# Kernel tuning notes

Measured on AMD Instinct MI355X. Metric: run time of the kernel, lower is better.

## Reference

```python
import jax, jax.numpy as jnp
import numpy as np

N_QUBITS = 4
N_LAYERS = 3
DIM = 2 ** N_QUBITS  # 16
BATCH = 524288

# CNOT ring permutations: wire 0 is the MOST significant bit (PennyLane default.qubit).
# CNOT(c,t) maps basis index j -> j ^ (target_mask * control_bit(j)); it is its own inverse,
# so new_state[:, j] = old_state[:, perm[j]] with the same perm.
_idx = np.arange(DIM)

def _cnot_perm(c, t):
    cbit = (_idx >> (N_QUBITS - 1 - c)) & 1
    return _idx ^ (cbit << (N_QUBITS - 1 - t))

CNOT_PERMS = [jnp.asarray(_cnot_perm(i, (i + 1) % N_QUBITS)) for i in range(N_QUBITS)]

# PauliZ signs per wire: +1 if bit is 0, -1 if bit is 1. Shape (4, 16).
Z_SIGNS = jnp.asarray(
    np.stack([1.0 - 2.0 * ((_idx >> (N_QUBITS - 1 - w)) & 1) for w in range(N_QUBITS)]).astype(np.float32)
)


def _bcast(v):
    # angle-derived factor: scalar stays scalar, batched (B,) -> (B,1,1)
    return v[:, None, None] if jnp.ndim(v) else v


def _apply_ry(state, wire, theta):
    # state: (B, 16) complex64; theta: scalar or (B,)
    B = state.shape[0]
    half = theta * 0.5
    c, s = _bcast(jnp.cos(half)), _bcast(jnp.sin(half))
    st = state.reshape(B, 2 ** wire, 2, 2 ** (N_QUBITS - 1 - wire))
    a0, a1 = st[:, :, 0, :], st[:, :, 1, :]
    return jnp.stack([c * a0 - s * a1, s * a0 + c * a1], axis=2).reshape(B, DIM)


def _apply_rz(state, wire, theta):
    # RZ = diag(e^{-i t/2}, e^{+i t/2})
    B = state.shape[0]
    half = theta * 0.5
    ch, sh = jnp.cos(half), jnp.sin(half)
    p0, p1 = _bcast(ch - 1j * sh), _bcast(ch + 1j * sh)
    st = state.reshape(B, 2 ** wire, 2, 2 ** (N_QUBITS - 1 - wire))
    return jnp.stack([p0 * st[:, :, 0, :], p1 * st[:, :, 1, :]], axis=2).reshape(B, DIM)


def setup_inputs() -> dict:
    key = jax.random.key(0)
    kx, kw = jax.random.split(key)
    x = jax.random.normal(kx, (BATCH, N_QUBITS), dtype=jnp.float32)
    weights = jax.random.normal(kw, (N_LAYERS, N_QUBITS, 2), dtype=jnp.float32) * 0.1
    return {"x": x, "weights": weights}


def reference(x, weights):
    B = x.shape[0]
    state = jnp.zeros((B, DIM), dtype=jnp.complex64).at[:, 0].set(1.0)
    # input-encoding RY rotations (batched angles)
    for i in range(N_QUBITS):
        state = _apply_ry(state, i, x[:, i])
    for layer in range(N_LAYERS):
        for i in range(N_QUBITS):
            state = state[:, CNOT_PERMS[i]]
        for i in range(N_QUBITS):
            state = _apply_ry(state, i, weights[layer, i, 0])
            state = _apply_rz(state, i, weights[layer, i, 1])
    probs = jnp.real(state) ** 2 + jnp.imag(state) ** 2  # (B, 16) float32
    return probs @ Z_SIGNS.T  # (B, 4) <Z_w> expectation values
```

## Files before the change

kernel.cpp:

```cpp
#include <hip/hip_runtime.h>

#define DIM 16
#define NQ 4
#define NL 3
#define VQC_BATCH 524288

typedef float v2f __attribute__((ext_vector_type(2)));
typedef const __attribute__((address_space(4))) v2f* cas_v2_p;

__global__ __launch_bounds__(64) void vqc_prep(const float* __restrict__ w,
                                               float* __restrict__ U) {
  const int col = threadIdx.x;
  if (col >= DIM) return;

  float cy[NL * NQ], sy[NL * NQ], cz[NL * NQ], sz[NL * NQ];
#pragma unroll
  for (int k = 0; k < NL * NQ; ++k) {
    const float ty = 0.5f * w[k * 2 + 0];
    const float tz = 0.5f * w[k * 2 + 1];
    cy[k] = __cosf(ty); sy[k] = __sinf(ty);
    cz[k] = __cosf(tz); sz[k] = __sinf(tz);
  }

  float sr[DIM], si[DIM];
#pragma unroll
  for (int k = 0; k < DIM; ++k) { sr[k] = (k == col) ? 1.f : 0.f; si[k] = 0.f; }

#pragma unroll
  for (int layer = 0; layer < NL; ++layer) {
#pragma unroll
    for (int c = 0; c < NQ; ++c) {
      const int t = (c + 1) & 3;
      float tr[DIM], ti[DIM];
#pragma unroll
      for (int idx = 0; idx < DIM; ++idx) {
        const int cbit = (idx >> (3 - c)) & 1;
        const int src = idx ^ (cbit << (3 - t));
        tr[idx] = sr[src]; ti[idx] = si[src];
      }
#pragma unroll
      for (int idx = 0; idx < DIM; ++idx) { sr[idx] = tr[idx]; si[idx] = ti[idx]; }
    }
#pragma unroll
    for (int q = 0; q < NQ; ++q) {
      const int m = 8 >> q;
      const int k = layer * NQ + q;
      const float c = cy[k], s = sy[k];
#pragma unroll
      for (int idx = 0; idx < DIM; ++idx) {
        if ((idx & m) == 0) {
          const int i1 = idx | m;
          const float a0r = sr[idx], a0i = si[idx];
          const float a1r = sr[i1], a1i = si[i1];
          sr[idx] = c * a0r - s * a1r;  si[idx] = c * a0i - s * a1i;
          sr[i1]  = s * a0r + c * a1r;  si[i1]  = s * a0i + c * a1i;
        }
      }
      const float ch = cz[k], sh = sz[k];
#pragma unroll
      for (int idx = 0; idx < DIM; ++idx) {
        const float ar = sr[idx], ai = si[idx];
        if (idx & m) { sr[idx] = ch * ar - sh * ai; si[idx] = ch * ai + sh * ar; }
        else         { sr[idx] = ch * ar + sh * ai; si[idx] = ch * ai - sh * ar; }
      }
    }
  }
  v2f* U2 = (v2f*)U;
#pragma unroll
  for (int j = 0; j < DIM; ++j) {
    v2f e; e.x = sr[j]; e.y = si[j];
    U2[j * DIM + col] = e;
  }
}

__global__ __launch_bounds__(256) void vqc_main(const float4* __restrict__ x4,
                                                const float* __restrict__ U,
                                                float4* __restrict__ out4) {
  const int b = blockIdx.x * 256 + threadIdx.x;
  const float4 xv = x4[b];

  const float s0 = __sinf(0.5f * xv.x), c0 = __cosf(0.5f * xv.x);
  const float s1 = __sinf(0.5f * xv.y), c1 = __cosf(0.5f * xv.y);
  const float s2 = __sinf(0.5f * xv.z), c2 = __cosf(0.5f * xv.z);
  const float s3 = __sinf(0.5f * xv.w), c3 = __cosf(0.5f * xv.w);

  float ab[4], cd[4];
  ab[0] = c0 * c1; ab[1] = c0 * s1; ab[2] = s0 * c1; ab[3] = s0 * s1;
  cd[0] = c2 * c3; cd[1] = c2 * s3; cd[2] = s2 * c3; cd[3] = s2 * s3;
  float sv[DIM];
#pragma unroll
  for (int hi = 0; hi < 4; ++hi)
#pragma unroll
    for (int lo = 0; lo < 4; ++lo)
      sv[hi * 4 + lo] = ab[hi] * cd[lo];

  cas_v2_p Uc = (cas_v2_p)(unsigned long long)U;
  v2f P[8];
#pragma unroll
  for (int t = 0; t < 8; ++t) {
    v2f acc0 = {0.f, 0.f}, acc1 = {0.f, 0.f};
#pragma unroll
    for (int i = 0; i < DIM; ++i) {
      const v2f sb = {sv[i], sv[i]};
      acc0 = __builtin_elementwise_fma(Uc[(2 * t) * DIM + i], sb, acc0);
      acc1 = __builtin_elementwise_fma(Uc[(2 * t + 1) * DIM + i], sb, acc1);
    }
    const v2f q0 = acc0 * acc0, q1 = acc1 * acc1;
    P[t].x = q0.x + q0.y;
    P[t].y = q1.x + q1.y;
  }

  const v2f C0 = P[0] + P[1], C1 = P[2] + P[3];
  const v2f C2 = P[4] + P[5], C3 = P[6] + P[7];
  const v2f C01 = C0 + C1, C23 = C2 + C3;
  const v2f S  = C01 + C23;
  const v2f D0 = C01 - C23;
  const v2f D1 = (C0 + C2) - (C1 + C3);
  const v2f Ea = P[0] + P[2], Eb = P[4] + P[6];
  const v2f Oa = P[1] + P[3], Ob = P[5] + P[7];
  const v2f D2 = (Ea + Eb) - (Oa + Ob);
  const float z0 = D0.x + D0.y;
  const float z1 = D1.x + D1.y;
  const float z2 = D2.x + D2.y;
  const float z3 = S.x - S.y;

  out4[b] = make_float4(z0, z1, z2, z3);
}

extern "C" void kernel_launch(void* const* d_in, const int* in_sizes, int n_in,
                              void* d_out, int out_size, void* d_ws, size_t ws_size,
                              hipStream_t stream) {
  const float* x = (const float*)d_in[0];
  const float* w = (const float*)d_in[1];
  float* U = (float*)d_ws;

  vqc_prep<<<1, 64, 0, stream>>>(w, U);
  vqc_main<<<VQC_BATCH / 256, 256, 0, stream>>>((const float4*)x, U,
                                                (float4*)d_out);
}
```

Before: 71.96 us.

## Fuse unitary construction into main kernel using wave shuffles and LDS

Drops the separate single-block prep kernel. Each block now rebuilds the 16x16 circuit unitary redundantly: one column per 16-lane group, with the gates applied through cross-lane shuffles, and the result stored in shared memory. The main matvec then reads the unitary from LDS as float4 rather than through constant-address-space loads. This removes a kernel launch and the serialized dependency on the prep kernel, at the cost of redundant per-block trig, shuffle work and a block barrier.

Measured after the change: 72.98 us. Within noise of the previous version (+1.4%).

```diff
diff --git a/kernel.cpp b/kernel.cpp
--- a/kernel.cpp
+++ b/kernel.cpp
@@ -6,77 +6,61 @@
 #define VQC_BATCH 524288
 
 typedef float v2f __attribute__((ext_vector_type(2)));
-typedef const __attribute__((address_space(4))) v2f* cas_v2_p;
 
-__global__ __launch_bounds__(64) void vqc_prep(const float* __restrict__ w,
-                                               float* __restrict__ U) {
-  const int col = threadIdx.x;
-  if (col >= DIM) return;
+__global__ __launch_bounds__(256) void vqc_fused(
+    const float4* __restrict__ x4, const float* __restrict__ w,
+    float4* __restrict__ out4) {
+  const int t = threadIdx.x;
+  const int r = t & 15;
+  const int c = t >> 4;
+  const int lane = t & 63;
+  const int grp = lane & 0x30;
 
-  float cy[NL * NQ], sy[NL * NQ], cz[NL * NQ], sz[NL * NQ];
-#pragma unroll
-  for (int k = 0; k < NL * NQ; ++k) {
-    const float ty = 0.5f * w[k * 2 + 0];
-    const float tz = 0.5f * w[k * 2 + 1];
-    cy[k] = __cosf(ty); sy[k] = __sinf(ty);
-    cz[k] = __cosf(tz); sz[k] = __sinf(tz);
-  }
-
-  float sr[DIM], si[DIM];
-#pragma unroll
-  for (int k = 0; k < DIM; ++k) { sr[k] = (k == col) ? 1.f : 0.f; si[k] = 0.f; }
+  float er = (r == c) ? 1.f : 0.f;
+  float ei = 0.f;
 
 #pragma unroll
   for (int layer = 0; layer < NL; ++layer) {
+    float cy[NQ], sy[NQ], cz[NQ], sz[NQ];
 #pragma unroll
-    for (int c = 0; c < NQ; ++c) {
-      const int t = (c + 1) & 3;
-      float tr[DIM], ti[DIM];
+    for (int q = 0; q < NQ; ++q) {
+      const int k = layer * NQ + q;
+      const float ty = 0.5f * w[2 * k];
+      const float tz = 0.5f * w[2 * k + 1];
+      cy[q] = __cosf(ty); sy[q] = __sinf(ty);
+      cz[q] = __cosf(tz); sz[q] = __sinf(tz);
+    }
 #pragma unroll
-      for (int idx = 0; idx < DIM; ++idx) {
-        const int cbit = (idx >> (3 - c)) & 1;
-        const int src = idx ^ (cbit << (3 - t));
-        tr[idx] = sr[src]; ti[idx] = si[src];
-      }
-#pragma unroll
-      for (int idx = 0; idx < DIM; ++idx) { sr[idx] = tr[idx]; si[idx] = ti[idx]; }
+    for (int i = 0; i < NQ; ++i) {
+      const int tq = (i + 1) & 3;
+      const int cbit = (r >> (3 - i)) & 1;
+      const int srcLane = grp | (r ^ (cbit << (3 - tq)));
+      er = __shfl(er, srcLane);
+      ei = __shfl(ei, srcLane);
     }
 #pragma unroll
     for (int q = 0; q < NQ; ++q) {
       const int m = 8 >> q;
-      const int k = layer * NQ + q;
-      const float c = cy[k], s = sy[k];
-#pragma unroll
-      for (int idx = 0; idx < DIM; ++idx) {
-        if ((idx & m) == 0) {
-          const int i1 = idx | m;
-          const float a0r = sr[idx], a0i = si[idx];
-          const float a1r = sr[i1], a1i = si[i1];
-          sr[idx] = c * a0r - s * a1r;  si[idx] = c * a0i - s * a1i;
-          sr[i1]  = s * a0r + c * a1r;  si[i1]  = s * a0i + c * a1i;
-        }
-      }
-      const float ch = cz[k], sh = sz[k];
-#pragma unroll
-      for (int idx = 0; idx < DIM; ++idx) {
-        const float ar = sr[idx], ai = si[idx];
-        if (idx & m) { sr[idx] = ch * ar - sh * ai; si[idx] = ch * ai + sh * ar; }
-        else         { sr[idx] = ch * ar + sh * ai; si[idx] = ch * ai - sh * ar; }
-      }
+      const float pr = __shfl_xor(er, m);
+      const float pi = __shfl_xor(ei, m);
+      const float sgy = (r & m) ? sy[q] : -sy[q];
+      er = cy[q] * er + sgy * pr;
+      ei = cy[q] * ei + sgy * pi;
+      const float sgz = (r & m) ? sz[q] : -sz[q];
+      const float ar = er, ai = ei;
+      er = cz[q] * ar - sgz * ai;
+      ei = cz[q] * ai + sgz * ar;
     }
   }
-  v2f* U2 = (v2f*)U;
-#pragma unroll
-  for (int j = 0; j < DIM; ++j) {
-    v2f e; e.x = sr[j]; e.y = si[j];
-    U2[j * DIM + col] = e;
+
+  __shared__ __align__(16) v2f Ush[DIM * DIM];
+  {
+    v2f e; e.x = er; e.y = ei;
+    Ush[r * DIM + c] = e;
   }
-}
+  __syncthreads();
 
-__global__ __launch_bounds__(256) void vqc_main(const float4* __restrict__ x4,
-                                                const float* __restrict__ U,
-                                                float4* __restrict__ out4) {
-  const int b = blockIdx.x * 256 + threadIdx.x;
+  const int b = blockIdx.x * 256 + t;
   const float4 xv = x4[b];
 
   const float s0 = __sinf(0.5f * xv.x), c0 = __cosf(0.5f * xv.x);
@@ -91,23 +75,31 @@
 #pragma unroll
   for (int hi = 0; hi < 4; ++hi)
 #pragma unroll
-    for (int lo = 0; lo < 4; ++lo)
-      sv[hi * 4 + lo] = ab[hi] * cd[lo];
+    for (int lo = 0; lo < 4; ++lo) sv[hi * 4 + lo] = ab[hi] * cd[lo];
 
-  cas_v2_p Uc = (cas_v2_p)(unsigned long long)U;
+  const float4* U4 = (const float4*)Ush;
   v2f P[8];
 #pragma unroll
-  for (int t = 0; t < 8; ++t) {
+  for (int tt = 0; tt < 8; ++tt) {
     v2f acc0 = {0.f, 0.f}, acc1 = {0.f, 0.f};
 #pragma unroll
-    for (int i = 0; i < DIM; ++i) {
-      const v2f sb = {sv[i], sv[i]};
-      acc0 = __builtin_elementwise_fma(Uc[(2 * t) * DIM + i], sb, acc0);
-      acc1 = __builtin_elementwise_fma(Uc[(2 * t + 1) * DIM + i], sb, acc1);
+    for (int p = 0; p < 8; ++p) {
+      const float4 u0 = U4[(2 * tt) * 8 + p];
+      const float4 u1 = U4[(2 * tt + 1) * 8 + p];
+      v2f sb0; sb0.x = sv[2 * p];     sb0.y = sv[2 * p];
+      v2f sb1; sb1.x = sv[2 * p + 1]; sb1.y = sv[2 * p + 1];
+      v2f a0; a0.x = u0.x; a0.y = u0.y;
+      v2f b0; b0.x = u0.z; b0.y = u0.w;
+      v2f a1; a1.x = u1.x; a1.y = u1.y;
+      v2f b1; b1.x = u1.z; b1.y = u1.w;
+      acc0 = __builtin_elementwise_fma(a0, sb0, acc0);
+      acc0 = __builtin_elementwise_fma(b0, sb1, acc0);
+      acc1 = __builtin_elementwise_fma(a1, sb0, acc1);
+      acc1 = __builtin_elementwise_fma(b1, sb1, acc1);
     }
     const v2f q0 = acc0 * acc0, q1 = acc1 * acc1;
-    P[t].x = q0.x + q0.y;
-    P[t].y = q1.x + q1.y;
+    P[tt].x = q0.x + q0.y;
+    P[tt].y = q1.x + q1.y;
   }
 
   const v2f C0 = P[0] + P[1], C1 = P[2] + P[3];
@@ -128,13 +120,10 @@
 }
 
 extern "C" void kernel_launch(void* const* d_in, const int* in_sizes, int n_in,
-                              void* d_out, int out_size, void* d_ws, size_t ws_size,
-                              hipStream_t stream) {
+                              void* d_out, int out_size, void* d_ws,
+                              size_t ws_size, hipStream_t stream) {
   const float* x = (const float*)d_in[0];
   const float* w = (const float*)d_in[1];
-  float* U = (float*)d_ws;
-
-  vqc_prep<<<1, 64, 0, stream>>>(w, U);
-  vqc_main<<<VQC_BATCH / 256, 256, 0, stream>>>((const float4*)x, U,
-                                                (float4*)d_out);
+  vqc_fused<<<VQC_BATCH / 256, 256, 0, stream>>>((const float4*)x, w,
+                                                 (float4*)d_out);
 }
```
